# Kernel optimization log

Measured on AMD Instinct MI355X. Metric: run time of the kernel, lower is better.

The kernel has to match this reference:

```python
import jax, jax.numpy as jnp
import numpy as np

N_NODES = 100000
N_EDGES = 3200000
HIDDEN = 128


def _linear_params(key, din, dout):
    s = 1.0 / np.sqrt(din)
    kw, kb = jax.random.split(key)
    W = jax.random.uniform(kw, (dout, din), minval=-s, maxval=s, dtype=jnp.float32)
    b = jax.random.uniform(kb, (dout,), minval=-s, maxval=s, dtype=jnp.float32)
    return W, b


def setup_inputs() -> dict:
    key = jax.random.key(0)
    ks = jax.random.split(key, 9)
    x = jax.random.normal(ks[0], (N_NODES, 5), dtype=jnp.float32)
    edge_index = jax.random.randint(ks[1], (2, N_EDGES), 0, N_NODES, dtype=jnp.int64)
    W1, b1 = _linear_params(ks[2], 5, 64)
    W2, b2 = _linear_params(ks[3], 64, HIDDEN)
    W3, b3 = _linear_params(ks[4], HIDDEN, HIDDEN)
    W4, b4 = _linear_params(ks[5], HIDDEN, HIDDEN)
    Wc1, bc1 = _linear_params(ks[6], HIDDEN, HIDDEN)
    Wc2, bc2 = _linear_params(ks[7], HIDDEN, HIDDEN)
    W5, b5 = _linear_params(ks[8], HIDDEN, 60)
    return {"x": x, "edge_index": edge_index,
            "W1": W1, "b1": b1, "W2": W2, "b2": b2,
            "W3": W3, "b3": b3, "W4": W4, "b4": b4,
            "Wc1": Wc1, "bc1": bc1, "Wc2": Wc2, "bc2": bc2,
            "W5": W5, "b5": b5}


def gcn_conv(x, edge_index, W, b):
    """GCNConv: self-loops + symmetric deg^-1/2 normalization."""
    n = x.shape[0]
    loop = jnp.arange(n, dtype=edge_index.dtype)
    src = jnp.concatenate([edge_index[0], loop])  # [E+N]
    dst = jnp.concatenate([edge_index[1], loop])  # [E+N]
    h = x @ W.T                                    # [N, H]
    ones = jnp.ones_like(dst, dtype=h.dtype)
    deg = jax.ops.segment_sum(ones, dst, num_segments=n)         # [N]
    dinv = jnp.where(deg > 0, jax.lax.rsqrt(deg), 0.0)
    norm = dinv[src] * dinv[dst]                                  # [E+N]
    msg = h[src] * norm[:, None]                                  # gather + scale
    out = jax.ops.segment_sum(msg, dst, num_segments=n)           # scatter-add
    return out + b


def reference(x, edge_index, W1, b1, W2, b2, W3, b3, W4, b4,
              Wc1, bc1, Wc2, bc2, W5, b5):
    h = jax.nn.relu(x @ W1.T + b1)
    h = jax.nn.relu(h @ W2.T + b2)
    h = jax.nn.relu(h @ W3.T + b3) + h
    h = jax.nn.relu(h @ W4.T + b4) + h
    h = jax.nn.relu(gcn_conv(h, edge_index, Wc1, bc1))
    h = jax.nn.relu(gcn_conv(h, edge_index, Wc2, bc2))
    return h @ W5.T + b5  # [N, 60]
```

## Files before the change

### kernel.cpp

```cpp
#include <hip/hip_runtime.h>
#include <hip/hip_fp16.h>

typedef __attribute__((ext_vector_type(8))) short bf16x8;
typedef __attribute__((ext_vector_type(4))) float f32x4;

__device__ __forceinline__ float frelu(float v){ return fmaxf(v, 0.f); }
__device__ __forceinline__ short f2bf(float f){
  unsigned u = __float_as_uint(f);
  unsigned r = (u + 0x7fffu + ((u>>16)&1u)) >> 16;
  return (short)r;
}
__device__ __forceinline__ float bf2f(short h){
  return __uint_as_float(((unsigned)(unsigned short)h) << 16);
}
__device__ __forceinline__ float4 addh4(float4 a, uint2 v){
  union { unsigned u; __half2 h; } p0, p1;
  p0.u = v.x; p1.u = v.y;
  a.x += __low2float(p0.h); a.y += __high2float(p0.h);
  a.z += __low2float(p1.h); a.w += __high2float(p1.h);
  return a;
}

template<int K, int BN, int COLS_REAL, int PRE, int EPI, int WRG, int WCG>
__global__ __launch_bounds__(512) void k_mgemm(const float* __restrict__ A,
    const float* __restrict__ W, const float* __restrict__ bpre,
    const float* __restrict__ bpost, const float* __restrict__ dscale,
    float* __restrict__ Out, int n)
{
  constexpr int BM = WRG*64;
  __shared__ __align__(16) short sAh[BM*32];
  __shared__ __align__(16) short sAl[BM*32];
  __shared__ __align__(16) short sWh[BN*32];
  __shared__ __align__(16) short sWl[BN*32];

  const int tid = threadIdx.x;
  const int nb0 = blockIdx.x * BM;
  const int l = tid & 63;
  const int w = tid >> 6;
  const int wr = w % WRG;
  const int wc = w / WRG;
  const int lrow = l & 15;
  const int koct = l >> 4;

  f32x4 acc[4][4];
  #pragma unroll
  for (int i=0;i<4;i++)
    #pragma unroll
    for (int j=0;j<4;j++) acc[i][j] = (f32x4){0.f,0.f,0.f,0.f};

  for (int kc = 0; kc < K/32; ++kc) {
    if (kc) __syncthreads();
    #pragma unroll
    for (int t = 0; t < BM/128; ++t) {
      int idx = tid + t*512;
      int row = idx >> 2, kq = idx & 3;
      int node = nb0 + row;
      float a[8];
      if (node < n) {
        const float* g = A + (size_t)node*K + kc*32 + kq*8;
        float4 v0 = *(const float4*)g;
        float4 v1 = *(const float4*)(g+4);
        a[0]=v0.x; a[1]=v0.y; a[2]=v0.z; a[3]=v0.w;
        a[4]=v1.x; a[5]=v1.y; a[6]=v1.z; a[7]=v1.w;
      } else {
        #pragma unroll
        for (int j=0;j<8;j++) a[j]=0.f;
      }
      if constexpr (PRE == 1) {
        const float* bp = bpre + kc*32 + kq*8;
        float4 b0 = *(const float4*)bp;
        float4 b1 = *(const float4*)(bp+4);
        a[0]=frelu(a[0]+b0.x); a[1]=frelu(a[1]+b0.y);
        a[2]=frelu(a[2]+b0.z); a[3]=frelu(a[3]+b0.w);
        a[4]=frelu(a[4]+b1.x); a[5]=frelu(a[5]+b1.y);
        a[6]=frelu(a[6]+b1.z); a[7]=frelu(a[7]+b1.w);
      }
      union { short s[8]; bf16x8 v; } ph, pl;
      #pragma unroll
      for (int j=0;j<8;j++) {
        short h = f2bf(a[j]);
        ph.s[j] = h;
        pl.s[j] = f2bf(a[j] - bf2f(h));
      }
      int byte = (row<<6) | (kq<<4);
      byte ^= (row&7)<<4;
      *(bf16x8*)((char*)sAh + byte) = ph.v;
      *(bf16x8*)((char*)sAl + byte) = pl.v;
    }
    if (BN*4 >= 512 || tid < BN*4) {
      int idx = tid;
      int c = idx >> 2, kq = idx & 3;
      float a[8];
      if (COLS_REAL == BN || c < COLS_REAL) {
        const float* g = W + (size_t)c*K + kc*32 + kq*8;
        float4 v0 = *(const float4*)g;
        float4 v1 = *(const float4*)(g+4);
        a[0]=v0.x; a[1]=v0.y; a[2]=v0.z; a[3]=v0.w;
        a[4]=v1.x; a[5]=v1.y; a[6]=v1.z; a[7]=v1.w;
      } else {
        #pragma unroll
        for (int j=0;j<8;j++) a[j]=0.f;
      }
      union { short s[8]; bf16x8 v; } ph, pl;
      #pragma unroll
      for (int j=0;j<8;j++) {
        short h = f2bf(a[j]);
        ph.s[j] = h;
        pl.s[j] = f2bf(a[j] - bf2f(h));
      }
      int byte = (c<<6) | (kq<<4);
      byte ^= (c&7)<<4;
      *(bf16x8*)((char*)sWh + byte) = ph.v;
      *(bf16x8*)((char*)sWl + byte) = pl.v;
    }
    __syncthreads();
    bf16x8 fah[4], fal[4], fwh[4], fwl[4];
    #pragma unroll
    for (int rf=0; rf<4; ++rf) {
      int row = wr*64 + rf*16 + lrow;
      int byte = (row<<6) | (koct<<4);
      byte ^= (row&7)<<4;
      fah[rf] = *(const bf16x8*)((const char*)sAh + byte);
      fal[rf] = *(const bf16x8*)((const char*)sAl + byte);
    }
    #pragma unroll
    for (int cf=0; cf<4; ++cf) {
      int c = wc*64 + cf*16 + lrow;
      int byte = (c<<6) | (koct<<4);
      byte ^= (c&7)<<4;
      fwh[cf] = *(const bf16x8*)((const char*)sWh + byte);
      fwl[cf] = *(const bf16x8*)((const char*)sWl + byte);
    }
    #pragma unroll
    for (int rf=0; rf<4; ++rf)
      #pragma unroll
      for (int cf=0; cf<4; ++cf) {
        acc[rf][cf] = __builtin_amdgcn_mfma_f32_16x16x32_bf16(fah[rf], fwh[cf], acc[rf][cf], 0,0,0);
        acc[rf][cf] = __builtin_amdgcn_mfma_f32_16x16x32_bf16(fah[rf], fwl[cf], acc[rf][cf], 0,0,0);
        acc[rf][cf] = __builtin_amdgcn_mfma_f32_16x16x32_bf16(fal[rf], fwh[cf], acc[rf][cf], 0,0,0);
      }
  }
  const int crow = (l >> 4) * 4;
  float bpc[4];
  if constexpr (EPI==1 || EPI==2 || EPI==3) {
    #pragma unroll
    for (int cf=0; cf<4; ++cf) {
      int col = wc*64 + cf*16 + (l & 15);
      bpc[cf] = (COLS_REAL == BN || col < COLS_REAL) ? bpost[col] : 0.f;
    }
  }
  #pragma unroll
  for (int rf=0; rf<4; ++rf) {
    #pragma unroll
    for (int reg=0; reg<4; ++reg) {
      int row = wr*64 + rf*16 + crow + reg;
      int node = nb0 + row;
      if (node >= n) continue;
      float ds = 1.f;
      if constexpr (EPI==4 || EPI==5) ds = dscale[node];
      #pragma unroll
      for (int cf=0; cf<4; ++cf) {
        int col = wc*64 + cf*16 + (l & 15);
        if (COLS_REAL != BN && col >= COLS_REAL) continue;
        float v = acc[rf][cf][reg];
        if constexpr (EPI==1) v += bpc[cf];
        if constexpr (EPI==2) v = frelu(v + bpc[cf]);
        if constexpr (EPI==3) v = frelu(v + bpc[cf]) + A[(size_t)node*K + col];
        if constexpr (EPI==4) v *= ds;
        if constexpr (EPI==5) {
          v *= ds;
          ((__half*)Out)[(size_t)node*COLS_REAL + col] = __float2half_rn(v);
        } else {
          Out[(size_t)node*COLS_REAL + col] = v;
        }
      }
    }
  }
}

__global__ __launch_bounds__(256) void k_wsplit(const float* __restrict__ W2,
    const float* __restrict__ W3, const float* __restrict__ W4,
    const float* __restrict__ Wc1, short* __restrict__ whi, short* __restrict__ wlo,
    int* __restrict__ bcnt)
{
  if (blockIdx.x == 0){
    bcnt[threadIdx.x] = 0;
    bcnt[threadIdx.x + 256] = 0;
  }
  int idx = blockIdx.x*256 + threadIdx.x;
  if (idx >= 57344) return;
  const float* src; int e, c, k, cbase;
  if (idx < 8192){ src=W2; e=idx; c=e>>6; k=e&63; cbase=0; }
  else if (idx < 24576){ src=W3; e=idx-8192; c=e>>7; k=e&127; cbase=8192; }
  else if (idx < 40960){ src=W4; e=idx-24576; c=e>>7; k=e&127; cbase=24576; }
  else { src=Wc1; e=idx-40960; c=e>>7; k=e&127; cbase=40960; }
  float v = src[e];
  short h = f2bf(v);
  short lo = f2bf(v - bf2f(h));
  int byte = ((c<<6) | ((k&31)<<1)) ^ ((c&7)<<4);
  int pos = cbase + (k>>5)*4096 + (byte>>1);
  whi[pos] = h; wlo[pos] = lo;
}

__global__ __launch_bounds__(256) void k_mega(const float* __restrict__ x,
    const float* __restrict__ W1, const float* __restrict__ b1,
    const float* __restrict__ b2, const float* __restrict__ b3,
    const float* __restrict__ b4, const short* __restrict__ whi,
    const short* __restrict__ wlo, const float* __restrict__ dinv,
    __half* __restrict__ tp1, int n)
{
  __shared__ __align__(16) short sWh[4096], sWl[4096];
  __shared__ __align__(16) short bAh[4096], bAl[4096];
  __shared__ __align__(16) short bBh[4096], bBl[4096];
  __shared__ float sx[160];
  __shared__ float sW1[320];
  __shared__ float sb1[64];
  const int tid = threadIdx.x;
  const int nb0 = blockIdx.x*32;

  if (tid < 160){ int row = tid/5, col = tid - row*5; int node = nb0 + row;
    sx[tid] = (node < n) ? x[(size_t)node*5 + col] : 0.f; }
  if (tid < 64) sb1[tid] = b1[tid];
  for (int i = tid; i < 320; i += 256) sW1[i] = W1[i];
  __syncthreads();

  {
    int row = tid >> 3, c0 = (tid & 7)*8;
    float xr[5];
    #pragma unroll
    for (int k=0;k<5;k++) xr[k] = sx[row*5+k];
    #pragma unroll
    for (int j=0;j<8;j++){
      int c = c0 + j;
      float a = sb1[c];
      #pragma unroll
      for (int k=0;k<5;k++) a = fmaf(xr[k], sW1[c*5+k], a);
      a = frelu(a);
      short h = f2bf(a), lo = f2bf(a - bf2f(h));
      int byte = ((c>>5)<<11) + ((((row<<6)|((c&31)<<1))) ^ ((row&7)<<4));
      *(short*)((char*)bAh + byte) = h;
      *(short*)((char*)bAl + byte) = lo;
    }
  }

  const int l = tid & 63, w = tid >> 6;
  const int wr = w >> 1, wc = w & 1;
  const int lrow = l & 15, koct = l >> 4;
  const int arow = wr*16 + lrow;
  const int abyteNoKc = ((arow<<6)|(koct<<4)) ^ ((arow&7)<<4);
  int wbyte[4];
  #pragma unroll
  for (int cf=0; cf<4; ++cf){
    int c = wc*64 + cf*16 + lrow;
    wbyte[cf] = ((c<<6)|(koct<<4)) ^ ((c&7)<<4);
  }
  f32x4 acc[4];
  float res[4][4];

  auto run_layer = [&](const short* inH, const short* inL, int woff, int nkc){
    #pragma unroll
    for (int cf=0; cf<4; ++cf) acc[cf] = (f32x4){0.f,0.f,0.f,0.f};
    for (int kc=0; kc<nkc; ++kc){
      __syncthreads();
      {
        const bf16x8* gh = (const bf16x8*)(whi + woff + kc*4096);
        const bf16x8* gl = (const bf16x8*)(wlo + woff + kc*4096);
        ((bf16x8*)sWh)[tid*2]   = gh[tid*2];
        ((bf16x8*)sWh)[tid*2+1] = gh[tid*2+1];
        ((bf16x8*)sWl)[tid*2]   = gl[tid*2];
        ((bf16x8*)sWl)[tid*2+1] = gl[tid*2+1];
      }
      __syncthreads();
      int ab = (kc<<11) + abyteNoKc;
      bf16x8 fah = *(const bf16x8*)((const char*)inH + ab);
      bf16x8 fal = *(const bf16x8*)((const char*)inL + ab);
      #pragma unroll
      for (int cf=0; cf<4; ++cf){
        bf16x8 fwh = *(const bf16x8*)((const char*)sWh + wbyte[cf]);
        bf16x8 fwl = *(const bf16x8*)((const char*)sWl + wbyte[cf]);
        acc[cf] = __builtin_amdgcn_mfma_f32_16x16x32_bf16(fah, fwh, acc[cf], 0,0,0);
        acc[cf] = __builtin_amdgcn_mfma_f32_16x16x32_bf16(fah, fwl, acc[cf], 0,0,0);
        acc[cf] = __builtin_amdgcn_mfma_f32_16x16x32_bf16(fal, fwh, acc[cf], 0,0,0);
      }
    }
  };
  auto store_buf = [&](short* outH, short* outL, int cf, int reg, float v){
    int row = wr*16 + koct*4 + reg;
    int col = wc*64 + cf*16 + lrow;
    short h = f2bf(v), lo = f2bf(v - bf2f(h));
    int byte = ((col>>5)<<11) + (((row<<6)|((col&31)<<1)) ^ ((row&7)<<4));
    *(short*)((char*)outH + byte) = h;
    *(short*)((char*)outL + byte) = lo;
  };

  run_layer(bAh, bAl, 0, 2);
  #pragma unroll
  for (int cf=0; cf<4; ++cf){
    float bb = b2[wc*64 + cf*16 + lrow];
    #pragma unroll
    for (int reg=0; reg<4; ++reg){
      float v = frelu(acc[cf][reg] + bb);
      res[cf][reg] = v;
      store_buf(bBh, bBl, cf, reg, v);
    }
  }
  run_layer(bBh, bBl, 8192, 4);
  #pragma unroll
  for (int cf=0; cf<4; ++cf){
    float bb = b3[wc*64 + cf*16 + lrow];
    #pragma unroll
    for (int reg=0; reg<4; ++reg){
      float v = frelu(acc[cf][reg] + bb) + res[cf][reg];
      res[cf][reg] = v;
      store_buf(bAh, bAl, cf, reg, v);
    }
  }
  run_layer(bAh, bAl, 24576, 4);
  #pragma unroll
  for (int cf=0; cf<4; ++cf){
    float bb = b4[wc*64 + cf*16 + lrow];
    #pragma unroll
    for (int reg=0; reg<4; ++reg){
      float v = frelu(acc[cf][reg] + bb) + res[cf][reg];
      store_buf(bBh, bBl, cf, reg, v);
    }
  }
  run_layer(bBh, bBl, 40960, 4);
  #pragma unroll
  for (int reg=0; reg<4; ++reg){
    int row = wr*16 + koct*4 + reg;
    int node = nb0 + row;
    float di = dinv[min(node, n-1)];
    #pragma unroll
    for (int cf=0; cf<4; ++cf){
      int col = wc*64 + cf*16 + lrow;
      if (node < n)
        tp1[(size_t)node*128 + col] = __float2half_rn(acc[cf][reg]*di);
    }
  }
}

__global__ __launch_bounds__(512) void k_bhist(const int* __restrict__ dst,
    int* __restrict__ bcnt, int E, int nbuck){
  __shared__ int l[512];
  int tid = threadIdx.x;
  if (tid < nbuck) l[tid]=0;
  __syncthreads();
  for (int e = blockIdx.x*512 + tid; e < E; e += gridDim.x*512)
    atomicAdd(&l[((unsigned)dst[e])>>8], 1);
  __syncthreads();
  if (tid < nbuck && l[tid]) atomicAdd(&bcnt[tid], l[tid]);
}
__global__ __launch_bounds__(512) void k_bscan(const int* __restrict__ bcnt,
    int* __restrict__ bbase, int* __restrict__ bcur, int nbuck){
  __shared__ int sc[512];
  int tid = threadIdx.x;
  int v = (tid<nbuck) ? bcnt[tid] : 0;
  sc[tid]=v; __syncthreads();
  for (int off=1; off<512; off<<=1){
    int t = (tid>=off)? sc[tid-off] : 0;
    __syncthreads();
    sc[tid]+=t;
    __syncthreads();
  }
  if (tid<nbuck){ bbase[tid]=sc[tid]-v; bcur[tid]=sc[tid]-v; }
  if (tid==nbuck-1) bbase[nbuck]=sc[tid];
}
__global__ __launch_bounds__(512) void k_bscatter(const int* __restrict__ src,
    const int* __restrict__ dst, int* __restrict__ bcur,
    unsigned* __restrict__ sorted, int E, int nbuck)
{
  __shared__ int lcnt[512];
  __shared__ int lbase[512];
  int tid = threadIdx.x;
  if (tid < nbuck) lcnt[tid]=0;
  __syncthreads();
  int e0 = blockIdx.x*8192;
  int e1 = min(e0+8192, E);
  for (int e = e0+tid; e < e1; e += 512)
    atomicAdd(&lcnt[((unsigned)dst[e])>>8], 1);
  __syncthreads();
  if (tid < nbuck) lbase[tid] = lcnt[tid] ? atomicAdd(&bcur[tid], lcnt[tid]) : 0;
  __syncthreads();
  if (tid < nbuck) lcnt[tid]=0;
  __syncthreads();
  for (int e = e0+tid; e < e1; e += 512){
    int d = dst[e];
    int k = ((unsigned)d)>>8;
    int pos = lbase[k] + atomicAdd(&lcnt[k], 1);
    sorted[pos] = (((unsigned)src[e])<<8) | ((unsigned)d & 255u);
  }
}
__global__ __launch_bounds__(512) void k_finesort(unsigned* __restrict__ sorted,
    const int* __restrict__ bbase, int* __restrict__ cend,
    float* __restrict__ dinv, int n, int* __restrict__ fb)
{
  constexpr int CAP = 16384;
  __shared__ int lsorted[CAP];
  __shared__ int cnt[256], cur[256], sc[256];
  const int k = blockIdx.x;
  const int base = bbase[k], endb = bbase[k+1];
  const int m = endb - base;
  const int node0 = k<<8;
  const int tid = threadIdx.x;
  if (tid<256) cnt[tid]=0;
  __syncthreads();
  for (int i=tid; i<m; i+=512) atomicAdd(&cnt[sorted[base+i]&255u], 1);
  __syncthreads();
  int v=0;
  if (tid<256){ v=cnt[tid]; sc[tid]=v; }
  __syncthreads();
  for (int off=1; off<256; off<<=1){
    int t=0;
    if (tid>=off && tid<256) t=sc[tid-off];
    __syncthreads();
    if (tid<256) sc[tid]+=t;
    __syncthreads();
  }
  if (tid<256){
    cur[tid]=sc[tid]-v;
    int node = node0 + tid;
    if (node < n){
      cend[node] = base + sc[tid];
      dinv[node] = rsqrtf((float)v + 1.0f);
    }
  }
  __syncthreads();
  if (m <= CAP){
    for (int i=tid; i<m; i+=512){
      unsigned p = sorted[base+i];
      int pos = atomicAdd(&cur[p&255u], 1);
      lsorted[pos] = (int)(p>>8);
    }
    __syncthreads();
    for (int i=tid; i<m; i+=512) sorted[base+i] = (unsigned)lsorted[i];
  } else {
    for (int i=tid; i<m; i+=512) fb[base+i] = (int)sorted[base+i];
    __syncthreads();
    for (int i=tid; i<m; i+=512){
      unsigned p = (unsigned)fb[base+i];
      int pos = atomicAdd(&cur[p&255u], 1);
      sorted[base+pos] = p>>8;
    }
  }
}

__global__ __launch_bounds__(256) void k_agg(const int* __restrict__ cend,
    const unsigned* __restrict__ srcs, const float* __restrict__ dinv,
    const __half* __restrict__ tp, float* __restrict__ out, int n)
{
  int node = blockIdx.x*4 + (threadIdx.x>>6);
  if (node >= n) return;
  const int lane = threadIdx.x & 63;
  const int sub = lane >> 5, li = lane & 31;
  const uint2* tpq = (const uint2*)tp;
  int beg = (node==0) ? 0 : cend[node-1];
  int end = cend[node];
  float4 acc = {0.f,0.f,0.f,0.f};
  int e = beg + sub;
  for (; e + 6 < end; e += 8){
    unsigned s0 = __builtin_nontemporal_load(srcs + e);
    unsigned s1 = __builtin_nontemporal_load(srcs + e + 2);
    unsigned s2 = __builtin_nontemporal_load(srcs + e + 4);
    unsigned s3 = __builtin_nontemporal_load(srcs + e + 6);
    uint2 v0 = tpq[(size_t)s0*32 + li];
    uint2 v1 = tpq[(size_t)s1*32 + li];
    uint2 v2 = tpq[(size_t)s2*32 + li];
    uint2 v3 = tpq[(size_t)s3*32 + li];
    acc = addh4(acc, v0);
    acc = addh4(acc, v1);
    acc = addh4(acc, v2);
    acc = addh4(acc, v3);
  }
  for (; e < end; e += 2){
    unsigned s = __builtin_nontemporal_load(srcs + e);
    uint2 v = tpq[(size_t)s*32 + li];
    acc = addh4(acc, v);
  }
  acc.x += __shfl_xor(acc.x, 32, 64);
  acc.y += __shfl_xor(acc.y, 32, 64);
  acc.z += __shfl_xor(acc.z, 32, 64);
  acc.w += __shfl_xor(acc.w, 32, 64);
  if (sub == 0){
    uint2 v = tpq[(size_t)node*32 + li];
    acc = addh4(acc, v);
    float di = dinv[node];
    float4 r = {acc.x*di, acc.y*di, acc.z*di, acc.w*di};
    *(float4*)(out + (size_t)node*128 + li*4) = r;
  }
}

extern "C" void kernel_launch(void* const* d_in, const int* in_sizes, int n_in,
                              void* d_out, int out_size, void* d_ws, size_t ws_size,
                              hipStream_t stream)
{
  const float* x   = (const float*)d_in[0];
  const int*   ei  = (const int*)d_in[1];
  const float *W1=(const float*)d_in[2],  *b1=(const float*)d_in[3];
  const float *W2=(const float*)d_in[4],  *b2=(const float*)d_in[5];
  const float *W3=(const float*)d_in[6],  *b3=(const float*)d_in[7];
  const float *W4=(const float*)d_in[8],  *b4=(const float*)d_in[9];
  const float *Wc1=(const float*)d_in[10],*bc1=(const float*)d_in[11];
  const float *Wc2=(const float*)d_in[12],*bc2=(const float*)d_in[13];
  const float *W5=(const float*)d_in[14], *b5=(const float*)d_in[15];
  float* out = (float*)d_out;

  const int n = in_sizes[0] / 5;
  const int E = in_sizes[1] / 2;
  const int* esrc = ei;
  const int* edst = ei + E;
  const int nbuck = (n + 255) >> 8;

  dim3 B256(256), B512(512);
  const int G256 = (n + 255)/256;
  const int G512 = (n + 511)/512;

  char* p = (char*)d_ws;
  float* hA    = (float*)p;           p += (size_t)n*128*4;
  float* hB    = (float*)p;           p += (size_t)n*128*4;
  float* dinv  = (float*)p;           p += (size_t)n*4;
  int*   cend  = (int*)p;             p += (size_t)n*4;
  unsigned* sortedp = (unsigned*)p;   p += (size_t)E*4;
  int*   bcnt  = (int*)p;             p += 512*4;
  int*   bbase = (int*)p;             p += 513*4;
  int*   bcur  = (int*)p;             p += 512*4;
  short* whi   = (short*)p;           p += 57344*2;
  short* wlo   = (short*)p;           p += 57344*2;

  k_wsplit<<<dim3(224), B256, 0, stream>>>(W2, W3, W4, Wc1, whi, wlo, bcnt);

  k_bhist<<<dim3(512), B512, 0, stream>>>(edst, bcnt, E, nbuck);
  k_bscan<<<dim3(1), B512, 0, stream>>>(bcnt, bbase, bcur, nbuck);
  k_bscatter<<<dim3((E + 8191)/8192), B512, 0, stream>>>(esrc, edst, bcur, sortedp, E, nbuck);
  k_finesort<<<dim3(nbuck), B512, 0, stream>>>(sortedp, bbase, cend, dinv, n, (int*)hA);

  k_mega<<<dim3((n + 31)/32), B256, 0, stream>>>(x, W1, b1, b2, b3, b4,
                                                 whi, wlo, dinv, (__half*)hA, n);
  k_agg<<<dim3((n+3)/4), B256, 0, stream>>>(cend, sortedp, dinv, (const __half*)hA, hB, n);

  k_mgemm<128,128,128,1,5,4,2><<<dim3(G256), B512, 0, stream>>>(hB, Wc2, bc1, nullptr, dinv, hA, n);
  k_agg<<<dim3((n+3)/4), B256, 0, stream>>>(cend, sortedp, dinv, (const __half*)hA, hB, n);

  k_mgemm<128,64,60,1,1,8,1><<<dim3(G512), B512, 0, stream>>>(hB, W5, bc2, b5, nullptr, out, n);
}
```

Baseline: 449.0 us.

## Fuse bias+relu into aggregation and store fp16 intermediates for GEMM inputs

The aggregation kernel now applies the conv bias and ReLU itself and writes its result in fp16 instead of fp32. The following GEMMs gain a PRE==2 mode that reads fp16 rows directly. This halves the intermediate write and read traffic between aggregation and GEMM, at the cost of fp16 rounding of the activations. Separately, the bucket histogram reads destinations as int4, and the fine-sort shared-memory capacity is reduced to 10240, which may raise occupancy but sends larger buckets to the global fallback path.

```diff
diff --git a/kernel.cpp b/kernel.cpp
--- a/kernel.cpp
+++ b/kernel.cpp
@@ -56,24 +56,36 @@
       int row = idx >> 2, kq = idx & 3;
       int node = nb0 + row;
       float a[8];
-      if (node < n) {
-        const float* g = A + (size_t)node*K + kc*32 + kq*8;
-        float4 v0 = *(const float4*)g;
-        float4 v1 = *(const float4*)(g+4);
-        a[0]=v0.x; a[1]=v0.y; a[2]=v0.z; a[3]=v0.w;
-        a[4]=v1.x; a[5]=v1.y; a[6]=v1.z; a[7]=v1.w;
+      if constexpr (PRE == 2) {
+        const __half* Ah = (const __half*)A;
+        union { uint4 u; __half2 h[4]; } v;
+        if (node < n) v.u = *(const uint4*)(Ah + (size_t)node*K + kc*32 + kq*8);
+        else { v.u.x=0u; v.u.y=0u; v.u.z=0u; v.u.w=0u; }
+        #pragma unroll
+        for (int j=0;j<4;j++){
+          a[2*j]   = __low2float(v.h[j]);
+          a[2*j+1] = __high2float(v.h[j]);
+        }
       } else {
-        #pragma unroll
-        for (int j=0;j<8;j++) a[j]=0.f;
-      }
-      if constexpr (PRE == 1) {
-        const float* bp = bpre + kc*32 + kq*8;
-        float4 b0 = *(const float4*)bp;
-        float4 b1 = *(const float4*)(bp+4);
-        a[0]=frelu(a[0]+b0.x); a[1]=frelu(a[1]+b0.y);
-        a[2]=frelu(a[2]+b0.z); a[3]=frelu(a[3]+b0.w);
-        a[4]=frelu(a[4]+b1.x); a[5]=frelu(a[5]+b1.y);
-        a[6]=frelu(a[6]+b1.z); a[7]=frelu(a[7]+b1.w);
+        if (node < n) {
+          const float* g = A + (size_t)node*K + kc*32 + kq*8;
+          float4 v0 = *(const float4*)g;
+          float4 v1 = *(const float4*)(g+4);
+          a[0]=v0.x; a[1]=v0.y; a[2]=v0.z; a[3]=v0.w;
+          a[4]=v1.x; a[5]=v1.y; a[6]=v1.z; a[7]=v1.w;
+        } else {
+          #pragma unroll
+          for (int j=0;j<8;j++) a[j]=0.f;
+        }
+        if constexpr (PRE == 1) {
+          const float* bp = bpre + kc*32 + kq*8;
+          float4 b0 = *(const float4*)bp;
+          float4 b1 = *(const float4*)(bp+4);
+          a[0]=frelu(a[0]+b0.x); a[1]=frelu(a[1]+b0.y);
+          a[2]=frelu(a[2]+b0.z); a[3]=frelu(a[3]+b0.w);
+          a[4]=frelu(a[4]+b1.x); a[5]=frelu(a[5]+b1.y);
+          a[6]=frelu(a[6]+b1.z); a[7]=frelu(a[7]+b1.w);
+        }
       }
       union { short s[8]; bf16x8 v; } ph, pl;
       #pragma unroll
@@ -346,7 +358,16 @@
   int tid = threadIdx.x;
   if (tid < nbuck) l[tid]=0;
   __syncthreads();
-  for (int e = blockIdx.x*512 + tid; e < E; e += gridDim.x*512)
+  const int E4 = E >> 2;
+  const int4* d4 = (const int4*)dst;
+  for (int i = blockIdx.x*512 + tid; i < E4; i += gridDim.x*512){
+    int4 v = d4[i];
+    atomicAdd(&l[((unsigned)v.x)>>8], 1);
+    atomicAdd(&l[((unsigned)v.y)>>8], 1);
+    atomicAdd(&l[((unsigned)v.z)>>8], 1);
+    atomicAdd(&l[((unsigned)v.w)>>8], 1);
+  }
+  for (int e = (E4<<2) + blockIdx.x*512 + tid; e < E; e += gridDim.x*512)
     atomicAdd(&l[((unsigned)dst[e])>>8], 1);
   __syncthreads();
   if (tid < nbuck && l[tid]) atomicAdd(&bcnt[tid], l[tid]);
@@ -395,7 +416,7 @@
     const int* __restrict__ bbase, int* __restrict__ cend,
     float* __restrict__ dinv, int n, int* __restrict__ fb)
 {
-  constexpr int CAP = 16384;
+  constexpr int CAP = 10240;
   __shared__ int lsorted[CAP];
   __shared__ int cnt[256], cur[256], sc[256];
   const int k = blockIdx.x;
@@ -447,7 +468,8 @@
 
 __global__ __launch_bounds__(256) void k_agg(const int* __restrict__ cend,
     const unsigned* __restrict__ srcs, const float* __restrict__ dinv,
-    const __half* __restrict__ tp, float* __restrict__ out, int n)
+    const float* __restrict__ bpre, const __half* __restrict__ tp,
+    __half* __restrict__ outh, int n)
 {
   int node = blockIdx.x*4 + (threadIdx.x>>6);
   if (node >= n) return;
@@ -485,8 +507,15 @@
     uint2 v = tpq[(size_t)node*32 + li];
     acc = addh4(acc, v);
     float di = dinv[node];
-    float4 r = {acc.x*di, acc.y*di, acc.z*di, acc.w*di};
-    *(float4*)(out + (size_t)node*128 + li*4) = r;
+    float4 bc = *(const float4*)(bpre + li*4);
+    float rx = frelu(fmaf(acc.x, di, bc.x));
+    float ry = frelu(fmaf(acc.y, di, bc.y));
+    float rz = frelu(fmaf(acc.z, di, bc.z));
+    float rw = frelu(fmaf(acc.w, di, bc.w));
+    union { __half2 h[2]; uint2 u; } o;
+    o.h[0] = __halves2half2(__float2half_rn(rx), __float2half_rn(ry));
+    o.h[1] = __halves2half2(__float2half_rn(rz), __float2half_rn(rw));
+    *(uint2*)(outh + (size_t)node*128 + li*4) = o.u;
   }
 }
 
@@ -536,10 +565,13 @@
 
   k_mega<<<dim3((n + 31)/32), B256, 0, stream>>>(x, W1, b1, b2, b3, b4,
                                                  whi, wlo, dinv, (__half*)hA, n);
-  k_agg<<<dim3((n+3)/4), B256, 0, stream>>>(cend, sortedp, dinv, (const __half*)hA, hB, n);
-
-  k_mgemm<128,128,128,1,5,4,2><<<dim3(G256), B512, 0, stream>>>(hB, Wc2, bc1, nullptr, dinv, hA, n);
-  k_agg<<<dim3((n+3)/4), B256, 0, stream>>>(cend, sortedp, dinv, (const __half*)hA, hB, n);
-
-  k_mgemm<128,64,60,1,1,8,1><<<dim3(G512), B512, 0, stream>>>(hB, W5, bc2, b5, nullptr, out, n);
-}
+  k_agg<<<dim3((n+3)/4), B256, 0, stream>>>(cend, sortedp, dinv, bc1,
+                                            (const __half*)hA, (__half*)hB, n);
+
+  k_mgemm<128,128,128,2,5,4,2><<<dim3(G256), B512, 0, stream>>>(hB, Wc2, nullptr, nullptr, dinv, hA, n);
+
+  k_agg<<<dim3((n+3)/4), B256, 0, stream>>>(cend, sortedp, dinv, bc2,
+                                            (const __half*)hA, (__half*)hB, n);
+
+  k_mgemm<128,64,60,2,1,8,1><<<dim3(G512), B512, 0, stream>>>(hB, W5, nullptr, b5, nullptr, out, n);
+}
```

Result: faster. 432.1 us (median of 2 runs) (-3.8%).
